# Optimization experiments

Measured on AMD Instinct MI355X. Metric: run time of the kernel, lower is better.

## Reference

```python
import jax, jax.numpy as jnp
import numpy as np

D = 127          # feature dim d
TD = D + 1       # token_dim = d + 1 = 128
H = D            # hidden_dim defaults to d
L = 2            # num_layers
EPS = 1e-6       # block eps
LN_EPS = 1e-5    # torch LayerNorm default


def _layernorm(x, w, b):
    m = jnp.mean(x, axis=-1, keepdims=True)
    v = jnp.mean(jnp.square(x - m), axis=-1, keepdims=True)
    return (x - m) * jax.lax.rsqrt(v + LN_EPS) * w + b


def _phi(x):
    return jax.nn.elu(x) + 1.0


def _gla_block(tokens, wq, wk, wv, wg_w, wg_b, wo, l1w, l1b, l2w, l2b):
    # tokens: (B, T, TD)
    x = _layernorm(tokens, l1w, l1b)
    Q = x @ wq.T                      # (B,T,H)
    K = x @ wk.T                      # (B,T,H)
    V = x @ wv.T                      # (B,T,TD)
    G = jax.nn.sigmoid(x @ wg_w.T + wg_b)
    Vg = V * G
    Qp = _phi(Q)
    Kp = _phi(K)
    # causal linear attention via cumulative outer-product state
    kv = jnp.einsum('bth,btm->bthm', Kp, Vg)   # (B,T,H,TD)
    S_kv = jnp.cumsum(kv, axis=1)
    S_k = jnp.cumsum(Kp, axis=1)
    numerator = jnp.einsum('bth,bthm->btm', Qp, S_kv)   # (B,T,TD)
    denom = jnp.maximum(jnp.einsum('bth,bth->bt', Qp, S_k), EPS)
    attn_out = numerator / denom[..., None]
    out = tokens + (attn_out @ wo.T) * 0.1
    return _layernorm(out, l2w, l2b)


def setup_inputs() -> dict:
    key = jax.random.key(0)
    ks = jax.random.split(key, 16)
    B, N = 2, 4095
    s = 0.02  # small xavier-ish gain used by the module
    inp = {
        'xs': jax.random.normal(ks[0], (B, N, D), jnp.float32),
        'ys': jax.random.normal(ks[1], (B, N), jnp.float32),
        'query_x': jax.random.normal(ks[2], (B, 1, D), jnp.float32),
        'Wq': jax.random.normal(ks[3], (L, H, TD), jnp.float32) * s,
        'Wk': jax.random.normal(ks[4], (L, H, TD), jnp.float32) * s,
        'Wv': jax.random.normal(ks[5], (L, TD, TD), jnp.float32) * s,
        'Wg_w': jax.random.normal(ks[6], (L, TD, TD), jnp.float32) * s,
        'Wg_b': jnp.zeros((L, TD), jnp.float32),
        'Wo': jax.random.normal(ks[7], (L, TD, TD), jnp.float32) * s,
        'ln1_w': jnp.ones((L, TD), jnp.float32),
        'ln1_b': jnp.zeros((L, TD), jnp.float32),
        'ln2_w': jnp.ones((L, TD), jnp.float32),
        'ln2_b': jnp.zeros((L, TD), jnp.float32),
        'pred_w': jax.random.normal(ks[8], (1, TD), jnp.float32) * 0.1,
    }
    return inp


def reference(xs, ys, query_x, Wq, Wk, Wv, Wg_w, Wg_b, Wo,
              ln1_w, ln1_b, ln2_w, ln2_b, pred_w):
    B = xs.shape[0]
    train_tokens = jnp.concatenate([xs, ys[..., None]], axis=-1)       # (B,N,TD)
    query_token = jnp.concatenate(
        [query_x, jnp.zeros((B, 1, 1), xs.dtype)], axis=-1)            # (B,1,TD)
    tokens = jnp.concatenate([train_tokens, query_token], axis=1)      # (B,T,TD)
    for l in range(L):
        tokens = _gla_block(tokens, Wq[l], Wk[l], Wv[l], Wg_w[l], Wg_b[l],
                            Wo[l], ln1_w[l], ln1_b[l], ln2_w[l], ln2_b[l])
    y_pred = tokens[:, -1, :] @ pred_w.T   # (B,1)
    return y_pred[:, 0]
```

## Files before the change

kernel.cpp:

```cpp
#include <hip/hip_runtime.h>
#include <hip/hip_bf16.h>

#define TT 4096
#define NCH 32
#define BB 2

__device__ float g_tok[(size_t)BB*TT*128];
__device__ float g_Qp [(size_t)BB*TT*128];
__device__ float g_Kp [(size_t)BB*TT*128];
__device__ float g_Vg [(size_t)BB*TT*128];
__device__ float g_Pv [(size_t)BB*TT*128];
__device__ float g_Pg [(size_t)BB*TT*128];
__device__ float g_Ssum[(size_t)BB*NCH*16384];
__device__ float g_Spre[(size_t)BB*NCH*16384];
__device__ float g_Sk [(size_t)BB*NCH*128];
__device__ float g_Skp[(size_t)BB*NCH*128];

__device__ __forceinline__ float phi_f(float x){ return x > 0.f ? x + 1.f : __expf(x); }
__device__ __forceinline__ float sigm_f(float x){ return 1.f/(1.f+__expf(-x)); }

__global__ __launch_bounds__(256) void k0_build(const float* __restrict__ xs,
                                                const float* __restrict__ ys,
                                                const float* __restrict__ qx){
  long e = (long)blockIdx.x * 256 + threadIdx.x;
  int col = (int)(e & 127);
  long r = e >> 7;
  int t = (int)(r & (TT-1));
  int b = (int)(r >> 12);
  float v;
  if (t < TT-1) {
    v = (col < 127) ? xs[((long)b*(TT-1) + t)*127 + col] : ys[(long)b*(TT-1) + t];
  } else {
    v = (col < 127) ? qx[(long)b*127 + col] : 0.f;
  }
  g_tok[e] = v;
}

__global__ __launch_bounds__(256) void k1b_gemm(
    const float* __restrict__ Wq, const float* __restrict__ Wk,
    const float* __restrict__ Wv, const float* __restrict__ Wg,
    const float* __restrict__ lnw, const float* __restrict__ lnb)
{
  __shared__ float xl[128*132];
  __shared__ float wt[128*132];
  int tid = threadIdx.x;
  int mat = blockIdx.x & 3;
  long row0 = (long)(blockIdx.x >> 2) * 128;
  const float* W = (mat==0) ? Wq : (mat==1) ? Wk : (mat==2) ? Wv : Wg;
  bool isQK = (mat < 2);
  for (int i=0;i<16;i++){
    int ts = (tid & 31) + 32*(i & 3);
    int hc = (tid >> 5) + 8*(i >> 2);
    int wr = isQK ? (ts < 127 ? ts : 126) : ts;
    float4 v = *(const float4*)(W + (long)wr*128 + hc*4);
    wt[(hc*4+0)*132+ts] = v.x;
    wt[(hc*4+1)*132+ts] = v.y;
    wt[(hc*4+2)*132+ts] = v.z;
    wt[(hc*4+3)*132+ts] = v.w;
  }
  {
    int row = tid >> 1, half = tid & 1;
    const float* src = g_tok + (row0 + row)*128 + half*64;
    float s1 = 0.f, s2 = 0.f;
    for (int u=0; u<16; u++){
      float4 v = *(const float4*)(src + u*4);
      s1 += v.x+v.y+v.z+v.w;
      s2 += v.x*v.x+v.y*v.y+v.z*v.z+v.w*v.w;
      *(float4*)&xl[row*132 + half*64 + u*4] = v;
    }
    s1 += __shfl_xor(s1, 1); s2 += __shfl_xor(s2, 1);
    float mean = s1*(1.f/128.f);
    float var  = s2*(1.f/128.f) - mean*mean;
    float rstd = rsqrtf(var + 1e-5f);
    for (int u=0; u<16; u++){
      int cc = half*64 + u*4;
      float4 v  = *(float4*)&xl[row*132 + cc];
      float4 w4 = *(const float4*)(lnw + cc);
      float4 b4 = *(const float4*)(lnb + cc);
      v.x = (v.x-mean)*rstd*w4.x + b4.x;
      v.y = (v.y-mean)*rstd*w4.y + b4.y;
      v.z = (v.z-mean)*rstd*w4.z + b4.z;
      v.w = (v.w-mean)*rstd*w4.w + b4.w;
      *(float4*)&xl[row*132 + cc] = v;
    }
  }
  __syncthreads();
  int g = tid >> 4, c = tid & 15;
  float acc[8][8];
  #pragma unroll
  for (int i=0;i<8;i++)
    #pragma unroll
    for (int j=0;j<8;j++) acc[i][j]=0.f;
  for (int k=0;k<128;k++){
    float xr[8];
    #pragma unroll
    for (int i=0;i<8;i++) xr[i] = xl[(g+16*i)*132 + k];
    float4 wa = *(const float4*)&wt[k*132 + c*4];
    float4 wb = *(const float4*)&wt[k*132 + 64 + c*4];
    float wc[8] = {wa.x,wa.y,wa.z,wa.w,wb.x,wb.y,wb.z,wb.w};
    #pragma unroll
    for (int i=0;i<8;i++)
      #pragma unroll
      for (int j=0;j<8;j++)
        acc[i][j] += xr[i]*wc[j];
  }
  if (isQK){
    float* dst = (mat==0) ? g_Qp : g_Kp;
    #pragma unroll
    for (int i=0;i<8;i++){
      long rr = row0 + g + 16*i;
      float v0[4], v1[4];
      #pragma unroll
      for (int j=0;j<4;j++) v0[j] = phi_f(acc[i][j]);
      #pragma unroll
      for (int j=0;j<4;j++){
        int col = 64 + c*4 + j;
        v1[j] = (col < 127) ? phi_f(acc[i][4+j]) : 0.f;
      }
      *(float4*)(dst + rr*128 + c*4)      = make_float4(v0[0],v0[1],v0[2],v0[3]);
      *(float4*)(dst + rr*128 + 64 + c*4) = make_float4(v1[0],v1[1],v1[2],v1[3]);
    }
  } else {
    float* dst = (mat==2) ? g_Pv : g_Pg;
    #pragma unroll
    for (int i=0;i<8;i++){
      long rr = row0 + g + 16*i;
      *(float4*)(dst + rr*128 + c*4)      = make_float4(acc[i][0],acc[i][1],acc[i][2],acc[i][3]);
      *(float4*)(dst + rr*128 + 64 + c*4) = make_float4(acc[i][4],acc[i][5],acc[i][6],acc[i][7]);
    }
  }
}

__global__ __launch_bounds__(256) void k1c_vg(const float* __restrict__ Wgb){
  long e = ((long)blockIdx.x*256 + threadIdx.x) * 4;
  int j = (int)(e & 127);
  float4 pv = *(const float4*)(g_Pv + e);
  float4 pg = *(const float4*)(g_Pg + e);
  float4 gb = *(const float4*)(Wgb + j);
  float4 o;
  o.x = pv.x * sigm_f(pg.x + gb.x);
  o.y = pv.y * sigm_f(pg.y + gb.y);
  o.z = pv.z * sigm_f(pg.z + gb.z);
  o.w = pv.w * sigm_f(pg.w + gb.w);
  *(float4*)(g_Vg + e) = o;
}

__global__ __launch_bounds__(256) void k2_chunksum()
{
  __shared__ float vgs[16][128];
  __shared__ float kps[16][32];
  int tid = threadIdx.x;
  int ht = blockIdx.x & 3;
  int c  = (blockIdx.x >> 2) & 31;
  int b  = blockIdx.x >> 7;
  int hl = tid >> 3, mg = tid & 7, m0 = mg << 4;
  int h  = ht*32 + hl;
  float acc[16];
  #pragma unroll
  for (int i=0;i<16;i++) acc[i]=0.f;
  float sk = 0.f;
  long base = ((long)b*TT + c*128)*128;
  for (int tb=0; tb<8; tb++){
    __syncthreads();
    { int e = tid*8; int ts = e >> 7; int cc = e & 127;
      const float* s = g_Vg + base + (long)(tb*16+ts)*128 + cc;
      *(float4*)&vgs[ts][cc]   = *(const float4*)s;
      *(float4*)&vgs[ts][cc+4] = *(const float4*)(s+4); }
    { int e = tid*2; int ts = e >> 5; int hh = e & 31;
      const float* s = g_Kp + base + (long)(tb*16+ts)*128 + ht*32 + hh;
      kps[ts][hh] = s[0]; kps[ts][hh+1] = s[1]; }
    __syncthreads();
    for (int ts=0; ts<16; ts++){
      float kp = kps[ts][hl];
      sk += kp;
      #pragma unroll
      for (int i=0;i<16;i++) acc[i] += kp * vgs[ts][m0+i];
    }
  }
  long so = (((long)b*NCH + c)*128 + h)*128 + m0;
  #pragma unroll
  for (int i=0;i<16;i+=4)
    *(float4*)(g_Ssum + so + i) = make_float4(acc[i],acc[i+1],acc[i+2],acc[i+3]);
  if (mg==0) g_Sk[((long)b*NCH + c)*128 + h] = sk;
}

__global__ __launch_bounds__(256) void k3_scan()
{
  int blk = blockIdx.x % 65;
  int b   = blockIdx.x / 65;
  if (blk < 64){
    int e = blk*256 + threadIdx.x;
    float a = 0.f;
    for (int c=0;c<NCH;c++){
      long idx = ((long)b*NCH + c)*16384 + e;
      g_Spre[idx] = a;
      a += g_Ssum[idx];
    }
  } else if (threadIdx.x < 128){
    int e = threadIdx.x;
    float a = 0.f;
    for (int c=0;c<NCH;c++){
      long idx = ((long)b*NCH + c)*128 + e;
      g_Skp[idx] = a;
      a += g_Sk[idx];
    }
  }
}

__global__ __launch_bounds__(256) void k4_fused(
    const float* __restrict__ Wo,
    const float* __restrict__ ln2w, const float* __restrict__ ln2b)
{
  __shared__ float spl[128*132];
  __shared__ float ktl[128*132];
  __shared__ float bufb[32*132];
  __shared__ float skl[128];
  int tid = threadIdx.x;
  int rq = blockIdx.x & 3;
  int c  = (blockIdx.x >> 2) & 31;
  int b  = blockIdx.x >> 7;
  int r0 = rq*32;
  long cbase = ((long)b*TT + c*128)*128;
  long sbase = ((long)b*NCH + c)*16384;

  for (int i=0;i<16;i++){
    int e = i*1024 + tid*4;
    int h = e >> 7, n = e & 127;
    *(float4*)&spl[h*132+n] = *(const float4*)(g_Spre + sbase + e);
  }
  if (tid < 128) skl[tid] = g_Skp[((long)b*NCH + c)*128 + tid];
  for (int i=0;i<4;i++){
    int e = i*1024 + tid*4;
    int row = e >> 7, cc = e & 127;
    *(float4*)&bufb[row*132+cc] = *(const float4*)(g_Qp + cbase + (long)(r0+row)*128 + cc);
  }
  for (int i=0;i<16;i++){
    int ts = (tid & 31) + 32*(i & 3);
    int hc = (tid >> 5) + 8*(i >> 2);
    float4 v = *(const float4*)(g_Kp + cbase + (long)ts*128 + hc*4);
    ktl[(hc*4+0)*132 + ts] = v.x;
    ktl[(hc*4+1)*132 + ts] = v.y;
    ktl[(hc*4+2)*132 + ts] = v.z;
    ktl[(hc*4+3)*132 + ts] = v.w;
  }
  __syncthreads();

  int rp = tid >> 4, cg = tid & 15;
  int rl0 = rp*2, rl1 = rp*2+1;
  int tq0 = r0 + rl0, tq1 = r0 + rl1;
  float acc2[2][8], a[2][8];
  #pragma unroll
  for (int r=0;r<2;r++)
    #pragma unroll
    for (int j=0;j<8;j++){ acc2[r][j]=0.f; a[r][j]=0.f; }
  float den0 = 0.f, den1 = 0.f;
  for (int h=0;h<128;h++){
    float q0 = bufb[rl0*132 + h];
    float q1 = bufb[rl1*132 + h];
    float sv = skl[h];
    den0 += q0*sv; den1 += q1*sv;
    float4 sa = *(const float4*)&spl[h*132 + cg*4];
    float4 sb = *(const float4*)&spl[h*132 + 64 + cg*4];
    float4 ka = *(const float4*)&ktl[h*132 + cg*4];
    float4 kb = *(const float4*)&ktl[h*132 + 64 + cg*4];
    acc2[0][0]+=q0*sa.x; acc2[0][1]+=q0*sa.y; acc2[0][2]+=q0*sa.z; acc2[0][3]+=q0*sa.w;
    acc2[0][4]+=q0*sb.x; acc2[0][5]+=q0*sb.y; acc2[0][6]+=q0*sb.z; acc2[0][7]+=q0*sb.w;
    acc2[1][0]+=q1*sa.x; acc2[1][1]+=q1*sa.y; acc2[1][2]+=q1*sa.z; acc2[1][3]+=q1*sa.w;
    acc2[1][4]+=q1*sb.x; acc2[1][5]+=q1*sb.y; acc2[1][6]+=q1*sb.z; acc2[1][7]+=q1*sb.w;
    a[0][0]+=q0*ka.x; a[0][1]+=q0*ka.y; a[0][2]+=q0*ka.z; a[0][3]+=q0*ka.w;
    a[0][4]+=q0*kb.x; a[0][5]+=q0*kb.y; a[0][6]+=q0*kb.z; a[0][7]+=q0*kb.w;
    a[1][0]+=q1*ka.x; a[1][1]+=q1*ka.y; a[1][2]+=q1*ka.z; a[1][3]+=q1*ka.w;
    a[1][4]+=q1*kb.x; a[1][5]+=q1*kb.y; a[1][6]+=q1*kb.z; a[1][7]+=q1*kb.w;
  }
  float dena0 = 0.f, dena1 = 0.f;
  #pragma unroll
  for (int j=0;j<8;j++){
    int ts = (j<4) ? (cg*4+j) : (64 + cg*4 + j-4);
    if (ts > tq0) a[0][j] = 0.f;
    if (ts > tq1) a[1][j] = 0.f;
    dena0 += a[0][j]; dena1 += a[1][j];
  }
  dena0 += __shfl_xor(dena0,1); dena1 += __shfl_xor(dena1,1);
  dena0 += __shfl_xor(dena0,2); dena1 += __shfl_xor(dena1,2);
  dena0 += __shfl_xor(dena0,4); dena1 += __shfl_xor(dena1,4);
  dena0 += __shfl_xor(dena0,8); dena1 += __shfl_xor(dena1,8);
  float inv0 = 1.f / fmaxf(den0 + dena0, 1e-6f);
  float inv1 = 1.f / fmaxf(den1 + dena1, 1e-6f);
  __syncthreads();
  *(float4*)&bufb[rl0*132 + cg*4]      = make_float4(a[0][0],a[0][1],a[0][2],a[0][3]);
  *(float4*)&bufb[rl0*132 + 64 + cg*4] = make_float4(a[0][4],a[0][5],a[0][6],a[0][7]);
  *(float4*)&bufb[rl1*132 + cg*4]      = make_float4(a[1][0],a[1][1],a[1][2],a[1][3]);
  *(float4*)&bufb[rl1*132 + 64 + cg*4] = make_float4(a[1][4],a[1][5],a[1][6],a[1][7]);
  for (int i=0;i<16;i++){
    int e = i*1024 + tid*4;
    *(float4*)&ktl[e] = *(const float4*)(g_Vg + cbase + e);
  }
  __syncthreads();
  for (int ts=0; ts<128; ts++){
    float a0 = bufb[rl0*132 + ts];
    float a1 = bufb[rl1*132 + ts];
    float4 va = *(const float4*)&ktl[ts*128 + cg*4];
    float4 vb = *(const float4*)&ktl[ts*128 + 64 + cg*4];
    acc2[0][0]+=a0*va.x; acc2[0][1]+=a0*va.y; acc2[0][2]+=a0*va.z; acc2[0][3]+=a0*va.w;
    acc2[0][4]+=a0*vb.x; acc2[0][5]+=a0*vb.y; acc2[0][6]+=a0*vb.z; acc2[0][7]+=a0*vb.w;
    acc2[1][0]+=a1*va.x; acc2[1][1]+=a1*va.y; acc2[1][2]+=a1*va.z; acc2[1][3]+=a1*va.w;
    acc2[1][4]+=a1*vb.x; acc2[1][5]+=a1*vb.y; acc2[1][6]+=a1*vb.z; acc2[1][7]+=a1*vb.w;
  }
  __syncthreads();
  *(float4*)&bufb[rl0*132 + cg*4]      = make_float4(acc2[0][0]*inv0,acc2[0][1]*inv0,acc2[0][2]*inv0,acc2[0][3]*inv0);
  *(float4*)&bufb[rl0*132 + 64 + cg*4] = make_float4(acc2[0][4]*inv0,acc2[0][5]*inv0,acc2[0][6]*inv0,acc2[0][7]*inv0);
  *(float4*)&bufb[rl1*132 + cg*4]      = make_float4(acc2[1][0]*inv1,acc2[1][1]*inv1,acc2[1][2]*inv1,acc2[1][3]*inv1);
  *(float4*)&bufb[rl1*132 + 64 + cg*4] = make_float4(acc2[1][4]*inv1,acc2[1][5]*inv1,acc2[1][6]*inv1,acc2[1][7]*inv1);
  for (int i=0;i<16;i++){
    int n  = (tid & 31) + 32*(i & 3);
    int mc = (tid >> 5) + 8*(i >> 2);
    float4 v = *(const float4*)(Wo + (long)n*128 + mc*4);
    ktl[(mc*4+0)*132 + n] = v.x;
    ktl[(mc*4+1)*132 + n] = v.y;
    ktl[(mc*4+2)*132 + n] = v.z;
    ktl[(mc*4+3)*132 + n] = v.w;
  }
  __syncthreads();
  float s[2][8];
  #pragma unroll
  for (int r=0;r<2;r++)
    #pragma unroll
    for (int j=0;j<8;j++) s[r][j]=0.f;
  for (int m=0;m<128;m++){
    float a0 = bufb[rl0*132 + m];
    float a1 = bufb[rl1*132 + m];
    float4 wa = *(const float4*)&ktl[m*132 + cg*4];
    float4 wb = *(const float4*)&ktl[m*132 + 64 + cg*4];
    s[0][0]+=a0*wa.x; s[0][1]+=a0*wa.y; s[0][2]+=a0*wa.z; s[0][3]+=a0*wa.w;
    s[0][4]+=a0*wb.x; s[0][5]+=a0*wb.y; s[0][6]+=a0*wb.z; s[0][7]+=a0*wb.w;
    s[1][0]+=a1*wa.x; s[1][1]+=a1*wa.y; s[1][2]+=a1*wa.z; s[1][3]+=a1*wa.w;
    s[1][4]+=a1*wb.x; s[1][5]+=a1*wb.y; s[1][6]+=a1*wb.z; s[1][7]+=a1*wb.w;
  }
  long trow0 = (long)b*TT + c*128 + tq0;
  long trow1 = (long)b*TT + c*128 + tq1;
  float outv[2][8];
  {
    float4 t0a = *(const float4*)(g_tok + trow0*128 + cg*4);
    float4 t0b = *(const float4*)(g_tok + trow0*128 + 64 + cg*4);
    float4 t1a = *(const float4*)(g_tok + trow1*128 + cg*4);
    float4 t1b = *(const float4*)(g_tok + trow1*128 + 64 + cg*4);
    outv[0][0]=t0a.x+0.1f*s[0][0]; outv[0][1]=t0a.y+0.1f*s[0][1];
    outv[0][2]=t0a.z+0.1f*s[0][2]; outv[0][3]=t0a.w+0.1f*s[0][3];
    outv[0][4]=t0b.x+0.1f*s[0][4]; outv[0][5]=t0b.y+0.1f*s[0][5];
    outv[0][6]=t0b.z+0.1f*s[0][6]; outv[0][7]=t0b.w+0.1f*s[0][7];
    outv[1][0]=t1a.x+0.1f*s[1][0]; outv[1][1]=t1a.y+0.1f*s[1][1];
    outv[1][2]=t1a.z+0.1f*s[1][2]; outv[1][3]=t1a.w+0.1f*s[1][3];
    outv[1][4]=t1b.x+0.1f*s[1][4]; outv[1][5]=t1b.y+0.1f*s[1][5];
    outv[1][6]=t1b.z+0.1f*s[1][6]; outv[1][7]=t1b.w+0.1f*s[1][7];
  }
  float s10=0.f, s20=0.f, s11=0.f, s21=0.f;
  #pragma unroll
  for (int j=0;j<8;j++){
    s10 += outv[0][j]; s20 += outv[0][j]*outv[0][j];
    s11 += outv[1][j]; s21 += outv[1][j]*outv[1][j];
  }
  s10 += __shfl_xor(s10,1); s20 += __shfl_xor(s20,1); s11 += __shfl_xor(s11,1); s21 += __shfl_xor(s21,1);
  s10 += __shfl_xor(s10,2); s20 += __shfl_xor(s20,2); s11 += __shfl_xor(s11,2); s21 += __shfl_xor(s21,2);
  s10 += __shfl_xor(s10,4); s20 += __shfl_xor(s20,4); s11 += __shfl_xor(s11,4); s21 += __shfl_xor(s21,4);
  s10 += __shfl_xor(s10,8); s20 += __shfl_xor(s20,8); s11 += __shfl_xor(s11,8); s21 += __shfl_xor(s21,8);
  float mean0 = s10*(1.f/128.f), var0 = s20*(1.f/128.f)-mean0*mean0, rstd0 = rsqrtf(var0+1e-5f);
  float mean1 = s11*(1.f/128.f), var1 = s21*(1.f/128.f)-mean1*mean1, rstd1 = rsqrtf(var1+1e-5f);
  #pragma unroll
  for (int half=0; half<2; half++){
    int n = half*64 + cg*4;
    float4 w4 = *(const float4*)(ln2w+n);
    float4 b4 = *(const float4*)(ln2b+n);
    float4 o0, o1;
    o0.x=(outv[0][half*4+0]-mean0)*rstd0*w4.x+b4.x;
    o0.y=(outv[0][half*4+1]-mean0)*rstd0*w4.y+b4.y;
    o0.z=(outv[0][half*4+2]-mean0)*rstd0*w4.z+b4.z;
    o0.w=(outv[0][half*4+3]-mean0)*rstd0*w4.w+b4.w;
    o1.x=(outv[1][half*4+0]-mean1)*rstd1*w4.x+b4.x;
    o1.y=(outv[1][half*4+1]-mean1)*rstd1*w4.y+b4.y;
    o1.z=(outv[1][half*4+2]-mean1)*rstd1*w4.z+b4.z;
    o1.w=(outv[1][half*4+3]-mean1)*rstd1*w4.w+b4.w;
    *(float4*)(g_tok + trow0*128 + n) = o0;
    *(float4*)(g_tok + trow1*128 + n) = o1;
  }
}

__global__ __launch_bounds__(128) void k5_pred(const float* __restrict__ pw,
                                               float* __restrict__ out){
  __shared__ float red[2];
  int b = blockIdx.x, tid = threadIdx.x;
  float v = g_tok[((long)b*TT + TT-1)*128 + tid] * pw[tid];
  #pragma unroll
  for (int off=1; off<64; off<<=1) v += __shfl_xor(v, off);
  if ((tid & 63) == 0) red[tid>>6] = v;
  __syncthreads();
  if (tid==0) out[b] = red[0] + red[1];
}

extern "C" void kernel_launch(void* const* d_in, const int* in_sizes, int n_in,
                              void* d_out, int out_size, void* d_ws, size_t ws_size,
                              hipStream_t stream)
{
  (void)in_sizes; (void)n_in; (void)out_size; (void)d_ws; (void)ws_size;
  const float* xs   = (const float*)d_in[0];
  const float* ys   = (const float*)d_in[1];
  const float* qx   = (const float*)d_in[2];
  const float* Wq   = (const float*)d_in[3];
  const float* Wk   = (const float*)d_in[4];
  const float* Wv   = (const float*)d_in[5];
  const float* Wgw  = (const float*)d_in[6];
  const float* Wgb  = (const float*)d_in[7];
  const float* Wo   = (const float*)d_in[8];
  const float* ln1w = (const float*)d_in[9];
  const float* ln1b = (const float*)d_in[10];
  const float* ln2w = (const float*)d_in[11];
  const float* ln2b = (const float*)d_in[12];
  const float* predw= (const float*)d_in[13];

  k0_build<<<4096, 256, 0, stream>>>(xs, ys, qx);

  for (int l=0; l<2; l++){
    const float* Wq_l  = Wq  + (size_t)l*127*128;
    const float* Wk_l  = Wk  + (size_t)l*127*128;
    const float* Wv_l  = Wv  + (size_t)l*128*128;
    const float* Wgw_l = Wgw + (size_t)l*128*128;
    const float* Wgb_l = Wgb + (size_t)l*128;
    const float* Wo_l  = Wo  + (size_t)l*128*128;
    const float* l1w = ln1w + (size_t)l*128;
    const float* l1b = ln1b + (size_t)l*128;
    const float* l2w = ln2w + (size_t)l*128;
    const float* l2b = ln2b + (size_t)l*128;

    k1b_gemm<<<256, 256, 0, stream>>>(Wq_l, Wk_l, Wv_l, Wgw_l, l1w, l1b);
    k1c_vg<<<1024, 256, 0, stream>>>(Wgb_l);
    k2_chunksum<<<256, 256, 0, stream>>>();
    k3_scan<<<130, 256, 0, stream>>>();
    k4_fused<<<256, 256, 0, stream>>>(Wo_l, l2w, l2b);
  }
  k5_pred<<<BB, 128, 0, stream>>>(predw, (float*)d_out);
}
```

Before: 244.3 us.

## Retile fused attention kernel to 4x4 per thread and vectorize chunk scan

```diff
diff --git a/kernel.cpp b/kernel.cpp
--- a/kernel.cpp
+++ b/kernel.cpp
@@ -186,23 +186,32 @@
 
 __global__ __launch_bounds__(256) void k3_scan()
 {
-  int blk = blockIdx.x % 65;
-  int b   = blockIdx.x / 65;
-  if (blk < 64){
-    int e = blk*256 + threadIdx.x;
-    float a = 0.f;
+  if (blockIdx.x < 32){
+    int gid = blockIdx.x*256 + threadIdx.x;
+    int b  = gid >> 12;
+    int e4 = gid & 4095;
+    long base = ((long)b*NCH)*16384 + (long)e4*4;
+    float4 v[NCH];
+    #pragma unroll
+    for (int c=0;c<NCH;c++)
+      v[c] = *(const float4*)(g_Ssum + base + (long)c*16384);
+    float4 run = make_float4(0.f,0.f,0.f,0.f);
+    #pragma unroll
     for (int c=0;c<NCH;c++){
-      long idx = ((long)b*NCH + c)*16384 + e;
-      g_Spre[idx] = a;
-      a += g_Ssum[idx];
-    }
-  } else if (threadIdx.x < 128){
-    int e = threadIdx.x;
-    float a = 0.f;
+      *(float4*)(g_Spre + base + (long)c*16384) = run;
+      run.x += v[c].x; run.y += v[c].y; run.z += v[c].z; run.w += v[c].w;
+    }
+  } else {
+    int b = threadIdx.x >> 7, h = threadIdx.x & 127;
+    long base = ((long)b*NCH)*128 + h;
+    float v[NCH];
+    #pragma unroll
+    for (int c=0;c<NCH;c++) v[c] = g_Sk[base + c*128];
+    float run = 0.f;
+    #pragma unroll
     for (int c=0;c<NCH;c++){
-      long idx = ((long)b*NCH + c)*128 + e;
-      g_Skp[idx] = a;
-      a += g_Sk[idx];
+      g_Skp[base + c*128] = run;
+      run += v[c];
     }
   }
 }
@@ -213,7 +222,7 @@
 {
   __shared__ float spl[128*132];
   __shared__ float ktl[128*132];
-  __shared__ float bufb[32*132];
+  __shared__ float bufb[32*133];
   __shared__ float skl[128];
   int tid = threadIdx.x;
   int rq = blockIdx.x & 3;
@@ -232,7 +241,7 @@
   for (int i=0;i<4;i++){
     int e = i*1024 + tid*4;
     int row = e >> 7, cc = e & 127;
-    *(float4*)&bufb[row*132+cc] = *(const float4*)(g_Qp + cbase + (long)(r0+row)*128 + cc);
+    *(float4*)&bufb[row*133+cc] = *(const float4*)(g_Qp + cbase + (long)(r0+row)*128 + cc);
   }
   for (int i=0;i<16;i++){
     int ts = (tid & 31) + 32*(i & 3);
@@ -245,72 +254,65 @@
   }
   __syncthreads();
 
-  int rp = tid >> 4, cg = tid & 15;
-  int rl0 = rp*2, rl1 = rp*2+1;
-  int tq0 = r0 + rl0, tq1 = r0 + rl1;
-  float acc2[2][8], a[2][8];
-  #pragma unroll
-  for (int r=0;r<2;r++)
-    #pragma unroll
-    for (int j=0;j<8;j++){ acc2[r][j]=0.f; a[r][j]=0.f; }
-  float den0 = 0.f, den1 = 0.f;
+  int rg = tid >> 5, cs = tid & 31;
+  int n0 = cs*4;
+  float acc2[4][4], a[4][4];
+  #pragma unroll
+  for (int r=0;r<4;r++)
+    #pragma unroll
+    for (int j=0;j<4;j++){ acc2[r][j]=0.f; a[r][j]=0.f; }
+  float den[4] = {0.f,0.f,0.f,0.f};
   for (int h=0;h<128;h++){
-    float q0 = bufb[rl0*132 + h];
-    float q1 = bufb[rl1*132 + h];
     float sv = skl[h];
-    den0 += q0*sv; den1 += q1*sv;
-    float4 sa = *(const float4*)&spl[h*132 + cg*4];
-    float4 sb = *(const float4*)&spl[h*132 + 64 + cg*4];
-    float4 ka = *(const float4*)&ktl[h*132 + cg*4];
-    float4 kb = *(const float4*)&ktl[h*132 + 64 + cg*4];
-    acc2[0][0]+=q0*sa.x; acc2[0][1]+=q0*sa.y; acc2[0][2]+=q0*sa.z; acc2[0][3]+=q0*sa.w;
-    acc2[0][4]+=q0*sb.x; acc2[0][5]+=q0*sb.y; acc2[0][6]+=q0*sb.z; acc2[0][7]+=q0*sb.w;
-    acc2[1][0]+=q1*sa.x; acc2[1][1]+=q1*sa.y; acc2[1][2]+=q1*sa.z; acc2[1][3]+=q1*sa.w;
-    acc2[1][4]+=q1*sb.x; acc2[1][5]+=q1*sb.y; acc2[1][6]+=q1*sb.z; acc2[1][7]+=q1*sb.w;
-    a[0][0]+=q0*ka.x; a[0][1]+=q0*ka.y; a[0][2]+=q0*ka.z; a[0][3]+=q0*ka.w;
-    a[0][4]+=q0*kb.x; a[0][5]+=q0*kb.y; a[0][6]+=q0*kb.z; a[0][7]+=q0*kb.w;
-    a[1][0]+=q1*ka.x; a[1][1]+=q1*ka.y; a[1][2]+=q1*ka.z; a[1][3]+=q1*ka.w;
-    a[1][4]+=q1*kb.x; a[1][5]+=q1*kb.y; a[1][6]+=q1*kb.z; a[1][7]+=q1*kb.w;
-  }
-  float dena0 = 0.f, dena1 = 0.f;
-  #pragma unroll
-  for (int j=0;j<8;j++){
-    int ts = (j<4) ? (cg*4+j) : (64 + cg*4 + j-4);
-    if (ts > tq0) a[0][j] = 0.f;
-    if (ts > tq1) a[1][j] = 0.f;
-    dena0 += a[0][j]; dena1 += a[1][j];
-  }
-  dena0 += __shfl_xor(dena0,1); dena1 += __shfl_xor(dena1,1);
-  dena0 += __shfl_xor(dena0,2); dena1 += __shfl_xor(dena1,2);
-  dena0 += __shfl_xor(dena0,4); dena1 += __shfl_xor(dena1,4);
-  dena0 += __shfl_xor(dena0,8); dena1 += __shfl_xor(dena1,8);
-  float inv0 = 1.f / fmaxf(den0 + dena0, 1e-6f);
-  float inv1 = 1.f / fmaxf(den1 + dena1, 1e-6f);
-  __syncthreads();
-  *(float4*)&bufb[rl0*132 + cg*4]      = make_float4(a[0][0],a[0][1],a[0][2],a[0][3]);
-  *(float4*)&bufb[rl0*132 + 64 + cg*4] = make_float4(a[0][4],a[0][5],a[0][6],a[0][7]);
-  *(float4*)&bufb[rl1*132 + cg*4]      = make_float4(a[1][0],a[1][1],a[1][2],a[1][3]);
-  *(float4*)&bufb[rl1*132 + 64 + cg*4] = make_float4(a[1][4],a[1][5],a[1][6],a[1][7]);
+    float4 s4 = *(const float4*)&spl[h*132 + n0];
+    float4 k4 = *(const float4*)&ktl[h*132 + n0];
+    #pragma unroll
+    for (int r=0;r<4;r++){
+      float qv = bufb[(4*rg+r)*133 + h];
+      den[r] += qv*sv;
+      acc2[r][0]+=qv*s4.x; acc2[r][1]+=qv*s4.y; acc2[r][2]+=qv*s4.z; acc2[r][3]+=qv*s4.w;
+      a[r][0]+=qv*k4.x; a[r][1]+=qv*k4.y; a[r][2]+=qv*k4.z; a[r][3]+=qv*k4.w;
+    }
+  }
+  float inv[4];
+  #pragma unroll
+  for (int r=0;r<4;r++){
+    int tq = r0 + 4*rg + r;
+    float dena = 0.f;
+    #pragma unroll
+    for (int j=0;j<4;j++){
+      if (n0 + j > tq) a[r][j] = 0.f;
+      dena += a[r][j];
+    }
+    dena += __shfl_xor(dena, 1);
+    dena += __shfl_xor(dena, 2);
+    dena += __shfl_xor(dena, 4);
+    dena += __shfl_xor(dena, 8);
+    dena += __shfl_xor(dena, 16);
+    inv[r] = 1.f / fmaxf(den[r] + dena, 1e-6f);
+  }
+  __syncthreads();
+  #pragma unroll
+  for (int r=0;r<4;r++)
+    *(float4*)&bufb[(4*rg+r)*133 + n0] = make_float4(a[r][0],a[r][1],a[r][2],a[r][3]);
   for (int i=0;i<16;i++){
     int e = i*1024 + tid*4;
     *(float4*)&ktl[e] = *(const float4*)(g_Vg + cbase + e);
   }
   __syncthreads();
   for (int ts=0; ts<128; ts++){
-    float a0 = bufb[rl0*132 + ts];
-    float a1 = bufb[rl1*132 + ts];
-    float4 va = *(const float4*)&ktl[ts*128 + cg*4];
-    float4 vb = *(const float4*)&ktl[ts*128 + 64 + cg*4];
-    acc2[0][0]+=a0*va.x; acc2[0][1]+=a0*va.y; acc2[0][2]+=a0*va.z; acc2[0][3]+=a0*va.w;
-    acc2[0][4]+=a0*vb.x; acc2[0][5]+=a0*vb.y; acc2[0][6]+=a0*vb.z; acc2[0][7]+=a0*vb.w;
-    acc2[1][0]+=a1*va.x; acc2[1][1]+=a1*va.y; acc2[1][2]+=a1*va.z; acc2[1][3]+=a1*va.w;
-    acc2[1][4]+=a1*vb.x; acc2[1][5]+=a1*vb.y; acc2[1][6]+=a1*vb.z; acc2[1][7]+=a1*vb.w;
-  }
-  __syncthreads();
-  *(float4*)&bufb[rl0*132 + cg*4]      = make_float4(acc2[0][0]*inv0,acc2[0][1]*inv0,acc2[0][2]*inv0,acc2[0][3]*inv0);
-  *(float4*)&bufb[rl0*132 + 64 + cg*4] = make_float4(acc2[0][4]*inv0,acc2[0][5]*inv0,acc2[0][6]*inv0,acc2[0][7]*inv0);
-  *(float4*)&bufb[rl1*132 + cg*4]      = make_float4(acc2[1][0]*inv1,acc2[1][1]*inv1,acc2[1][2]*inv1,acc2[1][3]*inv1);
-  *(float4*)&bufb[rl1*132 + 64 + cg*4] = make_float4(acc2[1][4]*inv1,acc2[1][5]*inv1,acc2[1][6]*inv1,acc2[1][7]*inv1);
+    float4 v4 = *(const float4*)&ktl[ts*128 + n0];
+    #pragma unroll
+    for (int r=0;r<4;r++){
+      float av = bufb[(4*rg+r)*133 + ts];
+      acc2[r][0]+=av*v4.x; acc2[r][1]+=av*v4.y; acc2[r][2]+=av*v4.z; acc2[r][3]+=av*v4.w;
+    }
+  }
+  __syncthreads();
+  #pragma unroll
+  for (int r=0;r<4;r++)
+    *(float4*)&bufb[(4*rg+r)*133 + n0] =
+      make_float4(acc2[r][0]*inv[r],acc2[r][1]*inv[r],acc2[r][2]*inv[r],acc2[r][3]*inv[r]);
   for (int i=0;i<16;i++){
     int n  = (tid & 31) + 32*(i & 3);
     int mc = (tid >> 5) + 8*(i >> 2);
@@ -321,66 +323,45 @@
     ktl[(mc*4+3)*132 + n] = v.w;
   }
   __syncthreads();
-  float s[2][8];
-  #pragma unroll
-  for (int r=0;r<2;r++)
-    #pragma unroll
-    for (int j=0;j<8;j++) s[r][j]=0.f;
+  float s[4][4];
+  #pragma unroll
+  for (int r=0;r<4;r++)
+    #pragma unroll
+    for (int j=0;j<4;j++) s[r][j]=0.f;
   for (int m=0;m<128;m++){
-    float a0 = bufb[rl0*132 + m];
-    float a1 = bufb[rl1*132 + m];
-    float4 wa = *(const float4*)&ktl[m*132 + cg*4];
-    float4 wb = *(const float4*)&ktl[m*132 + 64 + cg*4];
-    s[0][0]+=a0*wa.x; s[0][1]+=a0*wa.y; s[0][2]+=a0*wa.z; s[0][3]+=a0*wa.w;
-    s[0][4]+=a0*wb.x; s[0][5]+=a0*wb.y; s[0][6]+=a0*wb.z; s[0][7]+=a0*wb.w;
-    s[1][0]+=a1*wa.x; s[1][1]+=a1*wa.y; s[1][2]+=a1*wa.z; s[1][3]+=a1*wa.w;
-    s[1][4]+=a1*wb.x; s[1][5]+=a1*wb.y; s[1][6]+=a1*wb.z; s[1][7]+=a1*wb.w;
-  }
-  long trow0 = (long)b*TT + c*128 + tq0;
-  long trow1 = (long)b*TT + c*128 + tq1;
-  float outv[2][8];
-  {
-    float4 t0a = *(const float4*)(g_tok + trow0*128 + cg*4);
-    float4 t0b = *(const float4*)(g_tok + trow0*128 + 64 + cg*4);
-    float4 t1a = *(const float4*)(g_tok + trow1*128 + cg*4);
-    float4 t1b = *(const float4*)(g_tok + trow1*128 + 64 + cg*4);
-    outv[0][0]=t0a.x+0.1f*s[0][0]; outv[0][1]=t0a.y+0.1f*s[0][1];
-    outv[0][2]=t0a.z+0.1f*s[0][2]; outv[0][3]=t0a.w+0.1f*s[0][3];
-    outv[0][4]=t0b.x+0.1f*s[0][4]; outv[0][5]=t0b.y+0.1f*s[0][5];
-    outv[0][6]=t0b.z+0.1f*s[0][6]; outv[0][7]=t0b.w+0.1f*s[0][7];
-    outv[1][0]=t1a.x+0.1f*s[1][0]; outv[1][1]=t1a.y+0.1f*s[1][1];
-    outv[1][2]=t1a.z+0.1f*s[1][2]; outv[1][3]=t1a.w+0.1f*s[1][3];
-    outv[1][4]=t1b.x+0.1f*s[1][4]; outv[1][5]=t1b.y+0.1f*s[1][5];
-    outv[1][6]=t1b.z+0.1f*s[1][6]; outv[1][7]=t1b.w+0.1f*s[1][7];
-  }
-  float s10=0.f, s20=0.f, s11=0.f, s21=0.f;
-  #pragma unroll
-  for (int j=0;j<8;j++){
-    s10 += outv[0][j]; s20 += outv[0][j]*outv[0][j];
-    s11 += outv[1][j]; s21 += outv[1][j]*outv[1][j];
-  }
-  s10 += __shfl_xor(s10,1); s20 += __shfl_xor(s20,1); s11 += __shfl_xor(s11,1); s21 += __shfl_xor(s21,1);
-  s10 += __shfl_xor(s10,2); s20 += __shfl_xor(s20,2); s11 += __shfl_xor(s11,2); s21 += __shfl_xor(s21,2);
-  s10 += __shfl_xor(s10,4); s20 += __shfl_xor(s20,4); s11 += __shfl_xor(s11,4); s21 += __shfl_xor(s21,4);
-  s10 += __shfl_xor(s10,8); s20 += __shfl_xor(s20,8); s11 += __shfl_xor(s11,8); s21 += __shfl_xor(s21,8);
-  float mean0 = s10*(1.f/128.f), var0 = s20*(1.f/128.f)-mean0*mean0, rstd0 = rsqrtf(var0+1e-5f);
-  float mean1 = s11*(1.f/128.f), var1 = s21*(1.f/128.f)-mean1*mean1, rstd1 = rsqrtf(var1+1e-5f);
-  #pragma unroll
-  for (int half=0; half<2; half++){
-    int n = half*64 + cg*4;
-    float4 w4 = *(const float4*)(ln2w+n);
-    float4 b4 = *(const float4*)(ln2b+n);
-    float4 o0, o1;
-    o0.x=(outv[0][half*4+0]-mean0)*rstd0*w4.x+b4.x;
-    o0.y=(outv[0][half*4+1]-mean0)*rstd0*w4.y+b4.y;
-    o0.z=(outv[0][half*4+2]-mean0)*rstd0*w4.z+b4.z;
-    o0.w=(outv[0][half*4+3]-mean0)*rstd0*w4.w+b4.w;
-    o1.x=(outv[1][half*4+0]-mean1)*rstd1*w4.x+b4.x;
-    o1.y=(outv[1][half*4+1]-mean1)*rstd1*w4.y+b4.y;
-    o1.z=(outv[1][half*4+2]-mean1)*rstd1*w4.z+b4.z;
-    o1.w=(outv[1][half*4+3]-mean1)*rstd1*w4.w+b4.w;
-    *(float4*)(g_tok + trow0*128 + n) = o0;
-    *(float4*)(g_tok + trow1*128 + n) = o1;
+    float4 w4 = *(const float4*)&ktl[m*132 + n0];
+    #pragma unroll
+    for (int r=0;r<4;r++){
+      float av = bufb[(4*rg+r)*133 + m];
+      s[r][0]+=av*w4.x; s[r][1]+=av*w4.y; s[r][2]+=av*w4.z; s[r][3]+=av*w4.w;
+    }
+  }
+  float4 lw = *(const float4*)(ln2w+n0);
+  float4 lb = *(const float4*)(ln2b+n0);
+  #pragma unroll
+  for (int r=0;r<4;r++){
+    long trow = (long)b*TT + c*128 + r0 + 4*rg + r;
+    float4 t4 = *(const float4*)(g_tok + trow*128 + n0);
+    float o0 = t4.x + 0.1f*s[r][0];
+    float o1 = t4.y + 0.1f*s[r][1];
+    float o2 = t4.z + 0.1f*s[r][2];
+    float o3 = t4.w + 0.1f*s[r][3];
+    float s1 = o0+o1+o2+o3;
+    float s2 = o0*o0+o1*o1+o2*o2+o3*o3;
+    s1 += __shfl_xor(s1,1);  s2 += __shfl_xor(s2,1);
+    s1 += __shfl_xor(s1,2);  s2 += __shfl_xor(s2,2);
+    s1 += __shfl_xor(s1,4);  s2 += __shfl_xor(s2,4);
+    s1 += __shfl_xor(s1,8);  s2 += __shfl_xor(s2,8);
+    s1 += __shfl_xor(s1,16); s2 += __shfl_xor(s2,16);
+    float mean = s1*(1.f/128.f);
+    float var  = s2*(1.f/128.f) - mean*mean;
+    float rstd = rsqrtf(var + 1e-5f);
+    float4 o;
+    o.x = (o0-mean)*rstd*lw.x + lb.x;
+    o.y = (o1-mean)*rstd*lw.y + lb.y;
+    o.z = (o2-mean)*rstd*lw.z + lb.z;
+    o.w = (o3-mean)*rstd*lw.w + lb.w;
+    *(float4*)(g_tok + trow*128 + n0) = o;
   }
 }
 
@@ -433,7 +414,7 @@
     k1b_gemm<<<256, 256, 0, stream>>>(Wq_l, Wk_l, Wv_l, Wgw_l, l1w, l1b);
     k1c_vg<<<1024, 256, 0, stream>>>(Wgb_l);
     k2_chunksum<<<256, 256, 0, stream>>>();
-    k3_scan<<<130, 256, 0, stream>>>();
+    k3_scan<<<33, 256, 0, stream>>>();
     k4_fused<<<256, 256, 0, stream>>>(Wo_l, l2w, l2b);
   }
   k5_pred<<<BB, 128, 0, stream>>>(predw, (float*)d_out);
```

New measurement: 248.5 us. About the same (+1.7%).
